# Kernel tuning notes

Measured on AMD Instinct MI355X. Metric: run time of the kernel, lower is better.

## Reference

```python
import jax, jax.numpy as jnp
import numpy as np

EMBED_DIM = 1024
NUM_HEADS = 16
HEAD_DIM = EMBED_DIM // NUM_HEADS


def setup_inputs() -> dict:
    key = jax.random.key(0)
    k_x, k_qw, k_qb, k_ow, k_ob = jax.random.split(key, 5)
    B, T, C = 2, 2048, EMBED_DIM
    scale = 1.0 / np.sqrt(C)
    return {
        "x": jax.random.normal(k_x, (B, T, C), dtype=jnp.float32),
        "qkv_w": jax.random.normal(k_qw, (C, 3 * C), dtype=jnp.float32) * scale,
        "qkv_b": jax.random.normal(k_qb, (3 * C,), dtype=jnp.float32) * 0.02,
        "out_w": jax.random.normal(k_ow, (C, C), dtype=jnp.float32) * scale,
        "out_b": jax.random.normal(k_ob, (C,), dtype=jnp.float32) * 0.02,
    }


def reference(x, qkv_w, qkv_b, out_w, out_b):
    # x: (B, T, C). Causal masked multi-head self-attention (eval mode: dropout off).
    B, T, C = x.shape
    H, Dh = NUM_HEADS, HEAD_DIM
    qkv = x @ qkv_w + qkv_b                      # (B, T, 3C)
    qkv = qkv.reshape(B, T, 3, H, Dh)
    q = jnp.transpose(qkv[:, :, 0], (0, 2, 1, 3))  # (B, H, T, Dh)
    k = jnp.transpose(qkv[:, :, 1], (0, 2, 1, 3))
    v = jnp.transpose(qkv[:, :, 2], (0, 2, 1, 3))
    scores = jnp.einsum("bhqd,bhkd->bhqk", q, k) / np.sqrt(Dh)
    causal = jnp.tril(jnp.ones((T, T), dtype=bool))
    scores = jnp.where(causal[None, None], scores, -jnp.inf)
    attn = jax.nn.softmax(scores, axis=-1)        # (B, H, T, T)
    out = jnp.einsum("bhqk,bhkd->bhqd", attn, v)  # (B, H, T, Dh)
    out = jnp.transpose(out, (0, 2, 1, 3)).reshape(B, T, C)
    return out @ out_w + out_b
```

## Files before the change

### kernel.cpp

```cpp
#include <hip/hip_runtime.h>


typedef __bf16 bf16;
typedef __attribute__((ext_vector_type(4))) __bf16 bf16x4;
typedef __attribute__((ext_vector_type(8))) __bf16 bf16x8;
typedef __attribute__((ext_vector_type(4))) float f32x4;

#define T_SEQ 2048
#define NHEAD 16
#define QSCALE 0.1803368801111244f

__device__ __forceinline__ void async16(const bf16* g, const bf16* l) {
    __builtin_amdgcn_global_load_lds(
        (const __attribute__((address_space(1))) void*)g,
        (__attribute__((address_space(3))) void*)l, 16, 0, 0);
}

__global__ __launch_bounds__(256) void prep(
    const float* __restrict__ x, bf16* __restrict__ xb,
    const float* __restrict__ qkv_w, bf16* __restrict__ wbT,
    const float* __restrict__ out_w, bf16* __restrict__ owbT) {
    const int bid = blockIdx.x, tid = threadIdx.x;
    if (bid < 4096) {
        int i = (bid * 256 + tid) * 4;
        float4 v = *(const float4*)(x + i);
        bf16x4 o;
        o.x = (bf16)v.x; o.y = (bf16)v.y; o.z = (bf16)v.z; o.w = (bf16)v.w;
        *(bf16x4*)(xb + i) = o;
        return;
    }
    __shared__ float tile[32][33];
    const float* in;
    bf16* out;
    int K_, N_, b;
    if (bid < 7168) { b = bid - 4096; in = qkv_w; out = wbT; K_ = 1024; N_ = 3072; }
    else            { b = bid - 7168; in = out_w; out = owbT; K_ = 1024; N_ = 1024; }
    int k0 = (b & 31) * 32, n0 = (b >> 5) * 32;
    int tx = tid & 31, ty = tid >> 5;
    for (int r = 0; r < 32; r += 8)
        tile[ty + r][tx] = in[(k0 + ty + r) * N_ + n0 + tx];
    __syncthreads();
    for (int r = 0; r < 32; r += 8)
        out[(n0 + ty + r) * K_ + k0 + tx] = (bf16)tile[tx][ty + r];
}

__global__ __launch_bounds__(256) void gemm_qkv(
    const bf16* __restrict__ A, const bf16* __restrict__ Bt,
    const float* __restrict__ bias,
    bf16* __restrict__ Qo, bf16* __restrict__ Ko, bf16* __restrict__ Vt) {
    __shared__ __align__(16) bf16 As[128 * 32];
    __shared__ __align__(16) bf16 Bs[128 * 32];
    const int t = threadIdx.x;
    const int lane = t & 63, wave = t >> 6;
    const int l15 = lane & 15, quad = lane >> 4;
    const int wm = wave & 1, wn = wave >> 1;
    const int m0 = blockIdx.y * 128, n0 = blockIdx.x * 128;
    const int sec = n0 >> 10;

    f32x4 acc[4][4] = {};

    const bf16* ag = A + (m0 + (t >> 2)) * 1024 + (t & 3) * 8;
    const bf16* bg = Bt + (n0 + (t >> 2)) * 1024 + (t & 3) * 8;
    bf16* as0 = As + wave * 512;
    bf16* as1 = As + 2048 + wave * 512;
    bf16* bs0 = Bs + wave * 512;
    bf16* bs1 = Bs + 2048 + wave * 512;

    if (sec < 2) {
        for (int k0 = 0; k0 < 1024; k0 += 32) {
            async16(ag + k0, as0);
            async16(ag + 64 * 1024 + k0, as1);
            async16(bg + k0, bs0);
            async16(bg + 64 * 1024 + k0, bs1);
            __syncthreads();
            bf16x8 af[4], bfr[4];
            for (int i = 0; i < 4; i++)
                af[i] = *(const bf16x8*)(As + (wm * 64 + i * 16 + l15) * 32 + quad * 8);
            for (int j = 0; j < 4; j++)
                bfr[j] = *(const bf16x8*)(Bs + (wn * 64 + j * 16 + l15) * 32 + quad * 8);
            for (int j = 0; j < 4; j++)
                for (int i = 0; i < 4; i++)
                    acc[j][i] = __builtin_amdgcn_mfma_f32_16x16x32_bf16(bfr[j], af[i], acc[j][i], 0, 0, 0);
            __syncthreads();
        }
        bf16* dst = (sec == 0) ? Qo : Ko;
        const float sc = (sec == 0) ? QSCALE : 1.0f;
        for (int j = 0; j < 4; j++) {
            int col0 = n0 + wn * 64 + j * 16 + quad * 4;
            float4 bv = *(const float4*)(bias + col0);
            int c2 = col0 & 1023, h = c2 >> 6, d0 = c2 & 63;
            for (int i = 0; i < 4; i++) {
                int row = m0 + wm * 64 + i * 16 + l15;
                int b = row >> 11, tt = row & 2047;
                int bh = b * NHEAD + h;
                bf16x4 o;
                o[0] = (bf16)((acc[j][i][0] + bv.x) * sc);
                o[1] = (bf16)((acc[j][i][1] + bv.y) * sc);
                o[2] = (bf16)((acc[j][i][2] + bv.z) * sc);
                o[3] = (bf16)((acc[j][i][3] + bv.w) * sc);
                *(bf16x4*)(dst + (bh * T_SEQ + tt) * 64 + d0) = o;
            }
        }
    } else {
        for (int k0 = 0; k0 < 1024; k0 += 32) {
            async16(ag + k0, as0);
            async16(ag + 64 * 1024 + k0, as1);
            async16(bg + k0, bs0);
            async16(bg + 64 * 1024 + k0, bs1);
            __syncthreads();
            bf16x8 af[4], bfr[4];
            for (int i = 0; i < 4; i++)
                af[i] = *(const bf16x8*)(As + (wm * 64 + i * 16 + l15) * 32 + quad * 8);
            for (int j = 0; j < 4; j++)
                bfr[j] = *(const bf16x8*)(Bs + (wn * 64 + j * 16 + l15) * 32 + quad * 8);
            for (int i = 0; i < 4; i++)
                for (int j = 0; j < 4; j++)
                    acc[i][j] = __builtin_amdgcn_mfma_f32_16x16x32_bf16(af[i], bfr[j], acc[i][j], 0, 0, 0);
            __syncthreads();
        }
        for (int j = 0; j < 4; j++) {
            int col = n0 + wn * 64 + j * 16 + l15;
            float bv = bias[col];
            int c2 = col & 1023, h = c2 >> 6, d = c2 & 63;
            for (int i = 0; i < 4; i++) {
                int row0 = m0 + wm * 64 + i * 16 + quad * 4;
                int b = row0 >> 11, tt0 = row0 & 2047;
                int bh = b * NHEAD + h;
                bf16x4 o;
                for (int r = 0; r < 4; r++)
                    o[r] = (bf16)(acc[i][j][r] + bv);
                *(bf16x4*)(Vt + (bh * 64 + d) * T_SEQ + tt0) = o;
            }
        }
    }
}

#define PST 80
__global__ __launch_bounds__(256, 4) void attn(
    const bf16* __restrict__ Q, const bf16* __restrict__ K,
    const bf16* __restrict__ Vt, bf16* __restrict__ AO) {
    __shared__ __align__(16) bf16 Ks[2][64 * 64];
    __shared__ __align__(16) bf16 Vs[2][64 * 64];
    __shared__ __align__(16) bf16 Pa[4][16 * PST];
    const int tid = threadIdx.x;
    const int lane = tid & 63, wave = tid >> 6;
    const int l15 = lane & 15, quad = lane >> 4;
    const int xcdr = blockIdx.x & 7;
    const int i_ = blockIdx.x >> 3;
    const int bh = (xcdr << 2) | (i_ & 3);
    const int ti = i_ >> 2;
    const int qt = (ti & 1) ? (ti >> 1) : (31 - (ti >> 1));
    const int t0w = qt * 64 + wave * 16;

    const bf16* kp = K + bh * T_SEQ * 64;
    const bf16* vp = Vt + bh * 64 * T_SEQ;
    bf16* pw = &Pa[wave][0];
    const int b_ = bh >> 4, h_ = bh & 15;

    const int sx = (quad ^ (l15 & 7)) << 3;

    const bf16* qp = Q + (bh * T_SEQ + t0w) * 64;
    bf16x8 qf0 = *(const bf16x8*)(qp + l15 * 64 + quad * 8);
    bf16x8 qf1 = *(const bf16x8*)(qp + l15 * 64 + 32 + quad * 8);

    auto stage = [&](int kb, int b) {
        for (int i = 0; i < 2; i++) {
            int row = i * 32 + (tid >> 3), p = tid & 7;
            const bf16* ksrc = kp + (kb + row) * 64 + ((p ^ (row & 7)) << 3);
            async16(ksrc, &Ks[b][i * 2048 + wave * 512]);
            const bf16* vsrc = vp + row * T_SEQ + kb + ((p ^ (row & 7)) << 3);
            async16(vsrc, &Vs[b][i * 2048 + wave * 512]);
        }
    };

    f32x4 acc[4] = {};
    float lsum = 0.0f;

    const int C = qt + 1;
    stage(0, 0);
    for (int c = 0; c < C; c++) {
        __syncthreads();
        if (c + 1 < C) stage((c + 1) * 64, (c + 1) & 1);
        const bf16* ksb = &Ks[c & 1][0];
        const bf16* vsb = &Vs[c & 1][0];
        const bool dg = (c == qt);
        const int na = dg ? (wave + 1) : 4;

        f32x4 sc[4];
        for (int n = 0; n < 4; n++) {
            if (n < na) {
                const bf16* kbase = ksb + (n * 16 + l15) * 64;
                bf16x8 kf0 = *(const bf16x8*)(kbase + sx);
                bf16x8 kf1 = *(const bf16x8*)(kbase + (sx ^ 32));
                f32x4 z = {};
                z = __builtin_amdgcn_mfma_f32_16x16x32_bf16(kf0, qf0, z, 0, 0, 0);
                z = __builtin_amdgcn_mfma_f32_16x16x32_bf16(kf1, qf1, z, 0, 0, 0);
                sc[n] = z;
            }
        }
        for (int n = 0; n < 4; n++) {
            bf16x4 pv;
            if (n < na) {
                const bool dmask = dg && (n == na - 1);
                for (int r = 0; r < 4; r++) {
                    float v = sc[n][r];
                    if (dmask && (quad * 4 + r > l15)) v = -100000.0f;
                    float e = __builtin_amdgcn_exp2f(v);
                    lsum += e;
                    pv[r] = (bf16)e;
                }
            } else {
                pv[0] = pv[1] = pv[2] = pv[3] = (bf16)0.0f;
            }
            *(bf16x4*)(pw + l15 * PST + n * 16 + quad * 4) = pv;
        }
        __builtin_amdgcn_s_waitcnt(0xC07F);
        for (int g = 0; g < 2; g++) {
            bf16x8 pf = *(const bf16x8*)(pw + l15 * PST + g * 32 + quad * 8);
            for (int j = 0; j < 4; j++) {
                const bf16* vbase = vsb + (j * 16 + l15) * 64;
                bf16x8 vf = *(const bf16x8*)(vbase + (g ? (sx ^ 32) : sx));
                acc[j] = __builtin_amdgcn_mfma_f32_16x16x32_bf16(pf, vf, acc[j], 0, 0, 0);
            }
        }
    }

    lsum += __shfl_xor(lsum, 16);
    lsum += __shfl_xor(lsum, 32);
    float linv = 1.0f / lsum;

    bf16* aop = AO + (b_ * T_SEQ + t0w) * 1024 + h_ * 64;
    for (int r = 0; r < 4; r++) {
        float lr = __shfl(linv, quad * 4 + r, 16);
        for (int j = 0; j < 4; j++)
            aop[(quad * 4 + r) * 1024 + j * 16 + l15] = (bf16)(acc[j][r] * lr);
    }
}

__global__ __launch_bounds__(256) void gemm_out_k(
    const bf16* __restrict__ A, const bf16* __restrict__ Bt,
    const float* __restrict__ bias, float* __restrict__ out) {
    __shared__ __align__(16) bf16 As[64 * 32];
    __shared__ __align__(16) bf16 Bs[128 * 32];
    const int t = threadIdx.x;
    const int lane = t & 63, wave = t >> 6;
    const int l15 = lane & 15, quad = lane >> 4;
    const int wm = wave & 1, wn = wave >> 1;
    const int m0 = blockIdx.y * 64, n0 = blockIdx.x * 128;

    f32x4 acc[4][2] = {};

    const bf16* ag = A + (m0 + (t >> 2)) * 1024 + (t & 3) * 8;
    const bf16* bg = Bt + (n0 + (t >> 2)) * 1024 + (t & 3) * 8;
    bf16* as0 = As + wave * 512;
    bf16* bs0 = Bs + wave * 512;
    bf16* bs1 = Bs + 2048 + wave * 512;

    for (int k0 = 0; k0 < 1024; k0 += 32) {
        async16(ag + k0, as0);
        async16(bg + k0, bs0);
        async16(bg + 64 * 1024 + k0, bs1);
        __syncthreads();
        bf16x8 af[2], bfr[4];
        for (int i = 0; i < 2; i++)
            af[i] = *(const bf16x8*)(As + (wm * 32 + i * 16 + l15) * 32 + quad * 8);
        for (int j = 0; j < 4; j++)
            bfr[j] = *(const bf16x8*)(Bs + (wn * 64 + j * 16 + l15) * 32 + quad * 8);
        for (int j = 0; j < 4; j++)
            for (int i = 0; i < 2; i++)
                acc[j][i] = __builtin_amdgcn_mfma_f32_16x16x32_bf16(bfr[j], af[i], acc[j][i], 0, 0, 0);
        __syncthreads();
    }

    for (int j = 0; j < 4; j++) {
        int col0 = n0 + wn * 64 + j * 16 + quad * 4;
        float4 bv = *(const float4*)(bias + col0);
        for (int i = 0; i < 2; i++) {
            int row = m0 + wm * 32 + i * 16 + l15;
            float4 o;
            o.x = acc[j][i][0] + bv.x;
            o.y = acc[j][i][1] + bv.y;
            o.z = acc[j][i][2] + bv.z;
            o.w = acc[j][i][3] + bv.w;
            *(float4*)(out + row * 1024 + col0) = o;
        }
    }
}

extern "C" void kernel_launch(void* const* d_in, const int* in_sizes, int n_in,
                              void* d_out, int out_size, void* d_ws, size_t ws_size,
                              hipStream_t stream) {
    const float* x     = (const float*)d_in[0];
    const float* qkv_w = (const float*)d_in[1];
    const float* qkv_b = (const float*)d_in[2];
    const float* out_w = (const float*)d_in[3];
    const float* out_b = (const float*)d_in[4];
    float* out = (float*)d_out;

    char* ws = (char*)d_ws;
    bf16* xb   = (bf16*)(ws);
    bf16* wbT  = (bf16*)(ws + (8ull << 20));
    bf16* owbT = (bf16*)(ws + (14ull << 20));
    bf16* Qb   = (bf16*)(ws + (16ull << 20));
    bf16* Kb   = (bf16*)(ws + (24ull << 20));
    bf16* Vt   = (bf16*)(ws + (32ull << 20));
    bf16* AO   = (bf16*)(ws + (40ull << 20));

    prep<<<8192, 256, 0, stream>>>(x, xb, qkv_w, wbT, out_w, owbT);
    gemm_qkv<<<dim3(24, 32), 256, 0, stream>>>(xb, wbT, qkv_b, Qb, Kb, Vt);
    attn<<<1024, 256, 0, stream>>>(Qb, Kb, Vt, AO);
    gemm_out_k<<<dim3(8, 64), 256, 0, stream>>>(AO, owbT, out_b, out);
}
```

Baseline: 176.6 us.

## Double-buffer LDS tiles and XOR-swizzle layout in QKV and output GEMMs

Both projection GEMMs now use two LDS buffers. The async global-to-LDS copy for the next K-slice is issued right after the barrier, so it overlaps the MFMA work on the current slice, and one barrier per iteration is removed. The LDS tile layout is also XOR-swizzled on both the load and fragment-read sides to reduce bank conflicts on the bf16x8 reads. The cost is doubled LDS use per block, which may lower occupancy, plus more index arithmetic. The QKV GEMM's two branch loops are merged into one loop with the branch inside.

```diff
diff --git a/kernel.cpp b/kernel.cpp
--- a/kernel.cpp
+++ b/kernel.cpp
@@ -44,12 +44,13 @@
         out[(n0 + ty + r) * K_ + k0 + tx] = (bf16)tile[tx][ty + r];
 }
 
+
 __global__ __launch_bounds__(256) void gemm_qkv(
     const bf16* __restrict__ A, const bf16* __restrict__ Bt,
     const float* __restrict__ bias,
     bf16* __restrict__ Qo, bf16* __restrict__ Ko, bf16* __restrict__ Vt) {
-    __shared__ __align__(16) bf16 As[128 * 32];
-    __shared__ __align__(16) bf16 Bs[128 * 32];
+    __shared__ __align__(16) bf16 As[2][128 * 32];
+    __shared__ __align__(16) bf16 Bs[2][128 * 32];
     const int t = threadIdx.x;
     const int lane = t & 63, wave = t >> 6;
     const int l15 = lane & 15, quad = lane >> 4;
@@ -59,30 +60,48 @@
 
     f32x4 acc[4][4] = {};
 
-    const bf16* ag = A + (m0 + (t >> 2)) * 1024 + (t & 3) * 8;
-    const bf16* bg = Bt + (n0 + (t >> 2)) * 1024 + (t & 3) * 8;
-    bf16* as0 = As + wave * 512;
-    bf16* as1 = As + 2048 + wave * 512;
-    bf16* bs0 = Bs + wave * 512;
-    bf16* bs1 = Bs + 2048 + wave * 512;
-
-    if (sec < 2) {
-        for (int k0 = 0; k0 < 1024; k0 += 32) {
-            async16(ag + k0, as0);
-            async16(ag + 64 * 1024 + k0, as1);
-            async16(bg + k0, bs0);
-            async16(bg + 64 * 1024 + k0, bs1);
-            __syncthreads();
-            bf16x8 af[4], bfr[4];
-            for (int i = 0; i < 4; i++)
-                af[i] = *(const bf16x8*)(As + (wm * 64 + i * 16 + l15) * 32 + quad * 8);
-            for (int j = 0; j < 4; j++)
-                bfr[j] = *(const bf16x8*)(Bs + (wn * 64 + j * 16 + l15) * 32 + quad * 8);
+    const int sfat = t >> 3, sp = t & 7;
+    const int slg = sp ^ (sfat & 7);
+    const int smrow = sfat * 2 + (slg >> 2);
+    const int skoff = (slg & 3) << 3;
+    const bf16* ag = A + (m0 + smrow) * 1024 + skoff;
+    const bf16* bg = Bt + (n0 + smrow) * 1024 + skoff;
+    const int ldst = wave * 512;
+
+    auto stage = [&](int k0, int b) {
+        async16(ag + k0, &As[b][ldst]);
+        async16(ag + 64 * 1024 + k0, &As[b][2048 + ldst]);
+        async16(bg + k0, &Bs[b][ldst]);
+        async16(bg + 64 * 1024 + k0, &Bs[b][2048 + ldst]);
+    };
+
+    const int ffat = l15 >> 1;
+    const int fphys = (((l15 & 1) << 2) | quad) ^ (l15 >> 1);
+    const int foff = ffat * 64 + fphys * 8;
+
+    stage(0, 0);
+    for (int c = 0; c < 32; c++) {
+        __syncthreads();
+        if (c + 1 < 32) stage((c + 1) * 32, (c + 1) & 1);
+        const bf16* asb = &As[c & 1][0];
+        const bf16* bsb = &Bs[c & 1][0];
+        bf16x8 af[4], bfr[4];
+        for (int i = 0; i < 4; i++)
+            af[i] = *(const bf16x8*)(asb + (wm * 64 + i * 16) * 32 + foff);
+        for (int j = 0; j < 4; j++)
+            bfr[j] = *(const bf16x8*)(bsb + (wn * 64 + j * 16) * 32 + foff);
+        if (sec < 2) {
             for (int j = 0; j < 4; j++)
                 for (int i = 0; i < 4; i++)
                     acc[j][i] = __builtin_amdgcn_mfma_f32_16x16x32_bf16(bfr[j], af[i], acc[j][i], 0, 0, 0);
-            __syncthreads();
-        }
+        } else {
+            for (int i = 0; i < 4; i++)
+                for (int j = 0; j < 4; j++)
+                    acc[i][j] = __builtin_amdgcn_mfma_f32_16x16x32_bf16(af[i], bfr[j], acc[i][j], 0, 0, 0);
+        }
+    }
+
+    if (sec < 2) {
         bf16* dst = (sec == 0) ? Qo : Ko;
         const float sc = (sec == 0) ? QSCALE : 1.0f;
         for (int j = 0; j < 4; j++) {
@@ -102,22 +121,6 @@
             }
         }
     } else {
-        for (int k0 = 0; k0 < 1024; k0 += 32) {
-            async16(ag + k0, as0);
-            async16(ag + 64 * 1024 + k0, as1);
-            async16(bg + k0, bs0);
-            async16(bg + 64 * 1024 + k0, bs1);
-            __syncthreads();
-            bf16x8 af[4], bfr[4];
-            for (int i = 0; i < 4; i++)
-                af[i] = *(const bf16x8*)(As + (wm * 64 + i * 16 + l15) * 32 + quad * 8);
-            for (int j = 0; j < 4; j++)
-                bfr[j] = *(const bf16x8*)(Bs + (wn * 64 + j * 16 + l15) * 32 + quad * 8);
-            for (int i = 0; i < 4; i++)
-                for (int j = 0; j < 4; j++)
-                    acc[i][j] = __builtin_amdgcn_mfma_f32_16x16x32_bf16(af[i], bfr[j], acc[i][j], 0, 0, 0);
-            __syncthreads();
-        }
         for (int j = 0; j < 4; j++) {
             int col = n0 + wn * 64 + j * 16 + l15;
             float bv = bias[col];
@@ -240,8 +243,8 @@
 __global__ __launch_bounds__(256) void gemm_out_k(
     const bf16* __restrict__ A, const bf16* __restrict__ Bt,
     const float* __restrict__ bias, float* __restrict__ out) {
-    __shared__ __align__(16) bf16 As[64 * 32];
-    __shared__ __align__(16) bf16 Bs[128 * 32];
+    __shared__ __align__(16) bf16 As[2][64 * 32];
+    __shared__ __align__(16) bf16 Bs[2][128 * 32];
     const int t = threadIdx.x;
     const int lane = t & 63, wave = t >> 6;
     const int l15 = lane & 15, quad = lane >> 4;
@@ -250,26 +253,36 @@
 
     f32x4 acc[4][2] = {};
 
-    const bf16* ag = A + (m0 + (t >> 2)) * 1024 + (t & 3) * 8;
-    const bf16* bg = Bt + (n0 + (t >> 2)) * 1024 + (t & 3) * 8;
-    bf16* as0 = As + wave * 512;
-    bf16* bs0 = Bs + wave * 512;
-    bf16* bs1 = Bs + 2048 + wave * 512;
-
-    for (int k0 = 0; k0 < 1024; k0 += 32) {
-        async16(ag + k0, as0);
-        async16(bg + k0, bs0);
-        async16(bg + 64 * 1024 + k0, bs1);
+    const int sfat = t >> 3, sp = t & 7;
+    const int slg = sp ^ (sfat & 7);
+    const int smrow = sfat * 2 + (slg >> 2);
+    const int skoff = (slg & 3) << 3;
+    const bf16* ag = A + (m0 + smrow) * 1024 + skoff;
+    const bf16* bg = Bt + (n0 + smrow) * 1024 + skoff;
+    const int ldst = wave * 512;
+
+    auto stage = [&](int k0, int b) {
+        async16(ag + k0, &As[b][ldst]);
+        async16(bg + k0, &Bs[b][ldst]);
+        async16(bg + 64 * 1024 + k0, &Bs[b][2048 + ldst]);
+    };
+
+    const int foff = (l15 >> 1) * 64 + ((((l15 & 1) << 2) | quad) ^ (l15 >> 1)) * 8;
+
+    stage(0, 0);
+    for (int c = 0; c < 32; c++) {
         __syncthreads();
+        if (c + 1 < 32) stage((c + 1) * 32, (c + 1) & 1);
+        const bf16* asb = &As[c & 1][0];
+        const bf16* bsb = &Bs[c & 1][0];
         bf16x8 af[2], bfr[4];
         for (int i = 0; i < 2; i++)
-            af[i] = *(const bf16x8*)(As + (wm * 32 + i * 16 + l15) * 32 + quad * 8);
+            af[i] = *(const bf16x8*)(asb + (wm * 32 + i * 16) * 32 + foff);
         for (int j = 0; j < 4; j++)
-            bfr[j] = *(const bf16x8*)(Bs + (wn * 64 + j * 16 + l15) * 32 + quad * 8);
+            bfr[j] = *(const bf16x8*)(bsb + (wn * 64 + j * 16) * 32 + foff);
         for (int j = 0; j < 4; j++)
             for (int i = 0; i < 2; i++)
                 acc[j][i] = __builtin_amdgcn_mfma_f32_16x16x32_bf16(bfr[j], af[i], acc[j][i], 0, 0, 0);
-        __syncthreads();
     }
 
     for (int j = 0; j < 4; j++) {
```

After: 194.7 us. +10.2%, slower.
